# Kernel optimization log

Hardware: AMD Instinct MI355X
Metric: run time of the kernel (lower is better)

Reference implementation:

```python
import jax, jax.numpy as jnp
import numpy as np

MASK_FILL = -100.0


def setup_inputs() -> dict:
    key = jax.random.key(0)
    k1, k2, k3, k4 = jax.random.split(key, 4)
    B, S1, S2, D_IN, D_OUT = 8, 2048, 2048, 1024, 1024
    input1 = jax.random.normal(k1, (B, S1, D_IN), dtype=jnp.float32)
    input2 = jax.random.normal(k2, (B, S2, D_OUT), dtype=jnp.float32)
    input_mask = jax.random.randint(k3, (B, S1), 0, 2) > 0  # bool [B,S1]
    # kaiming_uniform-ish init scale for weight [out_features, in_features]
    bound = 1.0 / np.sqrt(D_IN)
    weight = jax.random.uniform(k4, (D_OUT, D_IN), dtype=jnp.float32,
                                minval=-bound, maxval=bound)
    return {"input1": input1, "input2": input2,
            "input_mask": input_mask, "weight": weight}


def reference(input1, input2, input_mask, weight):
    # out1 = F.linear(input1, weight): [B,S1,in] @ [in,out] -> [B,S1,out]
    out1 = jnp.einsum('bsd,od->bso', input1, weight)
    # scores: [B,S1,out] x [B,S2,out]^T -> [B,S1,S2]
    scores = jnp.einsum('bso,bto->bst', out1, input2)
    # out2[~input_mask] = -100 : mask is [B,S1], zeroes whole rows of scores
    scores = jnp.where(input_mask[:, :, None], scores, MASK_FILL)
    # softmax over S1 (dim=1), then attn^T @ input1 -> [B,S2,in]
    attn = jax.nn.softmax(scores, axis=1)
    satt = jnp.einsum('bst,bsd->btd', attn, input1)
    return satt
```

## Files before the change

### kernel.cpp

```cpp
#include <hip/hip_runtime.h>


typedef short s16x8 __attribute__((ext_vector_type(8)));
typedef float f32x4 __attribute__((ext_vector_type(4)));
typedef unsigned short u16;
typedef unsigned short u16x8 __attribute__((ext_vector_type(8)));
typedef _Float16 f16x8v __attribute__((ext_vector_type(8)));

#define B_ 8
#define S1_ 2048
#define S2_ 2048
#define D_ 1024

__device__ __forceinline__ float b2f(u16 u) {
  return __uint_as_float(((unsigned int)u) << 16);
}
__device__ __forceinline__ u16 f2b(float f) {
  unsigned int x = __float_as_uint(f);
  return (u16)((x + 0x7FFFu + ((x >> 16) & 1u)) >> 16);
}
__device__ __forceinline__ u16 f2h(float f) {
  _Float16 h = (_Float16)f;
  return __builtin_bit_cast(u16, h);
}
__device__ __forceinline__ float h2f(u16 u) {
  return (float)__builtin_bit_cast(_Float16, u);
}
__device__ __forceinline__ void gload16(const void* g, void* l) {
  __builtin_amdgcn_global_load_lds(
      (const __attribute__((address_space(1))) unsigned int*)g,
      (__attribute__((address_space(3))) unsigned int*)l, 16, 0, 0);
}

template <bool F16>
__device__ __forceinline__ f32x4 mfma16(s16x8 a, s16x8 b, f32x4 c) {
  if constexpr (F16)
    return __builtin_amdgcn_mfma_f32_16x16x32_f16(
        __builtin_bit_cast(f16x8v, a), __builtin_bit_cast(f16x8v, b), c, 0, 0,
        0);
  else
    return __builtin_amdgcn_mfma_f32_16x16x32_bf16(a, b, c, 0, 0, 0);
}


__global__ __launch_bounds__(256) void split_h_kernel(
    const float* __restrict__ in, u16* __restrict__ h, int n4) {
  int i = blockIdx.x * 256 + threadIdx.x;
  if (i >= n4) return;
  f32x4 v = ((const f32x4*)in)[i];
  ushort4 o;
  o.x = f2h(v[0]);
  o.y = f2h(v[1]);
  o.z = f2h(v[2]);
  o.w = f2h(v[3]);
  ((ushort4*)h)[i] = o;
}

__global__ __launch_bounds__(256) void zero_kernel(float* __restrict__ p,
                                                   int n) {
  int i = blockIdx.x * 256 + threadIdx.x;
  if (i < n) p[i] = 0.f;
}

template <int NSEG, int MODE, bool F16>
__global__ __launch_bounds__(512, 2) void gemm8(
    const u16* __restrict__ A0, const u16* __restrict__ A1,
    const u16* __restrict__ A2, const u16* __restrict__ B0,
    const u16* __restrict__ B1, const u16* __restrict__ B2,
    void* __restrict__ Cp, u16* __restrict__ C2, int K, int ldc, long sA,
    long sB, long sC, const int* __restrict__ mask, int maskStride,
    float* __restrict__ lvec, int lvecStride) {
  __shared__ __align__(16) u16 Abuf0[8192];
  __shared__ __align__(16) u16 Abuf1[8192];
  __shared__ __align__(16) u16 Abuf2[8192];
  __shared__ __align__(16) u16 Abuf3[8192];
  __shared__ __align__(16) u16 Bbuf0[8192];
  __shared__ __align__(16) u16 Bbuf1[8192];
  __shared__ __align__(16) u16 Bbuf2[8192];
  __shared__ __align__(16) u16 Bbuf3[8192];

  const int gx = gridDim.x, gy = gridDim.y;
  int flat = blockIdx.x + gx * (blockIdx.y + gy * blockIdx.z);
  const int total = gx * gy * (int)gridDim.z;
  const int cpx = total >> 3;
  flat = (flat & 7) * cpx + (flat >> 3);
  const int bx = flat % gx;
  const int rem0 = flat / gx;
  const int by = rem0 % gy;
  const int bz = rem0 / gy;

  const int tid = threadIdx.x;
  const int lane = tid & 63;
  const int wid = tid >> 6;
  const int wr = wid >> 2;
  const int wn = wid & 3;

  const int tps = K >> 5;
  const int NT = NSEG * tps;

  const int srow = tid >> 2;
  const int kch = (tid & 3) ^ ((srow >> 1) & 3);
  const long aRow1 = (long)(by * 256 + srow) * K + kch * 8;
  const long aRow2 = (long)(by * 256 + srow + 128) * K + kch * 8;
  const long bRow1 = (long)(bx * 256 + srow) * K + kch * 8;
  const long bRow2 = (long)(bx * 256 + srow + 128) * K + kch * 8;

  const u16* aBase0 = A0 + (long)bz * sA;
  const u16* bBase0 = B0 + (long)bz * sB;
  const u16* aBase1 = (NSEG > 1) ? A1 + (long)bz * sA : aBase0;
  const u16* bBase1 = (NSEG > 1) ? B1 + (long)bz * sB : bBase0;
  const u16* aBase2 = (NSEG > 2) ? A2 + (long)bz * sA : aBase0;
  const u16* bBase2 = (NSEG > 2) ? B2 + (long)bz * sB : bBase0;

  const int lr = lane & 15;
  const int kg = lane >> 4;
  const int arow0 = wr * 128 + lr;
  const int aOffU = arow0 * 32 + (kg ^ ((arow0 >> 1) & 3)) * 8;
  const int brow0 = wn * 64 + lr;
  const int bOffU = brow0 * 32 + (kg ^ ((brow0 >> 1) & 3)) * 8;

  const f32x4 z4 = {0.f, 0.f, 0.f, 0.f};
  f32x4 acc[8][4];
#pragma unroll
  for (int i = 0; i < 8; ++i)
#pragma unroll
    for (int j = 0; j < 4; ++j) acc[i][j] = z4;

  int s_rem = 0, s_seg = 0;
  const u16* aS = aBase0;
  const u16* bS = bBase0;

#define STAGE_AB(DA_, DB_)                                                   \
  {                                                                          \
    gload16(aS + aRow1 + s_rem * 32, &DA_[wid * 512]);                       \
    gload16(aS + aRow2 + s_rem * 32, &DA_[wid * 512 + 4096]);                \
    gload16(bS + bRow1 + s_rem * 32, &DB_[wid * 512]);                       \
    gload16(bS + bRow2 + s_rem * 32, &DB_[wid * 512 + 4096]);                \
    if (++s_rem == tps) {                                                    \
      s_rem = 0;                                                             \
      ++s_seg;                                                               \
      aS = (s_seg == 1) ? aBase1 : aBase2;                                   \
      bS = (s_seg == 1) ? bBase1 : bBase2;                                   \
    }                                                                        \
  }

  STAGE_AB(Abuf0, Bbuf0);
  STAGE_AB(Abuf1, Bbuf1);
  STAGE_AB(Abuf2, Bbuf2);
  asm volatile("s_waitcnt vmcnt(8)" ::: "memory");
  __builtin_amdgcn_s_barrier();

#define ITER(AS_, BS_, DA_, DB_, VM_, STG_)                                  \
  {                                                                          \
    s16x8 a0[4], a1[4], bfr[4];                                              \
    _Pragma("unroll") for (int m_ = 0; m_ < 4; ++m_) a0[m_] =                \
        *(const s16x8*)&AS_[aOffU + m_ * 512];                               \
    _Pragma("unroll") for (int n_ = 0; n_ < 4; ++n_) bfr[n_] =               \
        *(const s16x8*)&BS_[bOffU + n_ * 512];                               \
    _Pragma("unroll") for (int m_ = 0; m_ < 4; ++m_) a1[m_] =                \
        *(const s16x8*)&AS_[aOffU + (m_ + 4) * 512];                         \
    if (STG_) {                                                              \
      gload16(aS + aRow1 + s_rem * 32, &DA_[wid * 512]);                     \
      gload16(aS + aRow2 + s_rem * 32, &DA_[wid * 512 + 4096]);              \
    }                                                                        \
    asm volatile("" ::: "memory");                                           \
    __builtin_amdgcn_s_barrier();                                            \
    __builtin_amdgcn_sched_barrier(0);                                       \
    __builtin_amdgcn_s_setprio(1);                                           \
    _Pragma("unroll") for (int m_ = 0; m_ < 4; ++m_)                         \
        _Pragma("unroll") for (int n_ = 0; n_ < 4; ++n_) acc[m_][n_] =       \
            mfma16<F16>(a0[m_], bfr[n_], acc[m_][n_]);                       \
    __builtin_amdgcn_s_setprio(0);                                           \
    if (STG_) {                                                              \
      gload16(bS + bRow1 + s_rem * 32, &DB_[wid * 512]);                     \
      gload16(bS + bRow2 + s_rem * 32, &DB_[wid * 512 + 4096]);              \
      if (++s_rem == tps) {                                                  \
        s_rem = 0;                                                           \
        ++s_seg;                                                             \
        aS = (s_seg == 1) ? aBase1 : aBase2;                                 \
        bS = (s_seg == 1) ? bBase1 : bBase2;                                 \
      }                                                                      \
    }                                                                        \
    asm volatile("s_waitcnt " VM_ ::: "memory");                             \
    __builtin_amdgcn_s_barrier();                                            \
    __builtin_amdgcn_sched_barrier(0);                                       \
    __builtin_amdgcn_s_setprio(1);                                           \
    _Pragma("unroll") for (int m_ = 0; m_ < 4; ++m_)                         \
        _Pragma("unroll") for (int n_ = 0; n_ < 4; ++n_) acc[m_ + 4][n_] =   \
            mfma16<F16>(a1[m_], bfr[n_], acc[m_ + 4][n_]);                   \
    __builtin_amdgcn_s_setprio(0);                                           \
  }

  for (int t = 0; t < NT - 4; t += 4) {
    ITER(Abuf0, Bbuf0, Abuf3, Bbuf3, "vmcnt(8)", true);
    ITER(Abuf1, Bbuf1, Abuf0, Bbuf0, "vmcnt(8)", true);
    ITER(Abuf2, Bbuf2, Abuf1, Bbuf1, "vmcnt(8)", true);
    ITER(Abuf3, Bbuf3, Abuf2, Bbuf2, "vmcnt(8)", true);
  }
  ITER(Abuf0, Bbuf0, Abuf3, Bbuf3, "vmcnt(8)", true);
  ITER(Abuf1, Bbuf1, Abuf0, Bbuf0, "vmcnt(4)", false);
  ITER(Abuf2, Bbuf2, Abuf1, Bbuf1, "vmcnt(0)", false);
  ITER(Abuf3, Bbuf3, Abuf2, Bbuf2, "vmcnt(0)", false);

#undef ITER
#undef STAGE_AB

  const int row0 = by * 256 + wr * 128 + kg * 4;
  const int col0 = bx * 256 + wn * 64 + lr;

  if (MODE == 0) {
    u16* Ch = (u16*)Cp;
    u16* Cl = C2;
#pragma unroll
    for (int m = 0; m < 8; ++m)
#pragma unroll
      for (int n = 0; n < 4; ++n)
#pragma unroll
        for (int r = 0; r < 4; ++r) {
          float v = acc[m][n][r];
          long idx = (long)(row0 + m * 16 + r) * ldc + (col0 + n * 16);
          if (F16) {
            u16 h = f2h(v);
            Ch[idx] = h;
            Cl[idx] = f2h(v - h2f(h));
          } else {
            u16 h = f2b(v);
            Ch[idx] = h;
            Cl[idx] = f2b(v - b2f(h));
          }
        }
  } else if (MODE == 1) {
    u16* Cb = (u16*)Cp + (long)bz * sC;
    const int* mb = mask + (long)bz * maskStride;
    float* lvout = lvec + (long)bz * lvecStride;
    int mcol[4];
#pragma unroll
    for (int n = 0; n < 4; ++n) mcol[n] = mb[col0 + n * 16];
#pragma unroll
    for (int m = 0; m < 8; ++m)
#pragma unroll
      for (int r = 0; r < 4; ++r) {
        float rv = 0.f;
#pragma unroll
        for (int n = 0; n < 4; ++n) {
          float v = acc[m][n][r];
          v = mcol[n] ? __expf(v - 100.0f) : 0.0f;
          Cb[(long)(row0 + m * 16 + r) * ldc + (col0 + n * 16)] = f2b(v);
          rv += v;
        }
        rv += __shfl_xor(rv, 1, 16);
        rv += __shfl_xor(rv, 2, 16);
        rv += __shfl_xor(rv, 4, 16);
        rv += __shfl_xor(rv, 8, 16);
        if (lr == 0) atomicAdd(&lvout[row0 + m * 16 + r], rv);
      }
  } else {
    float* Cb = (float*)Cp + (long)bz * sC;
    const float* lb = lvec + (long)bz * lvecStride;
#pragma unroll
    for (int m = 0; m < 8; ++m) {
      float sc[4];
#pragma unroll
      for (int r = 0; r < 4; ++r) {
        float dv = lb[row0 + m * 16 + r];
        sc[r] = (dv > 0.0f) ? 1.0f / dv : 0.0f;
      }
#pragma unroll
      for (int n = 0; n < 4; ++n)
#pragma unroll
        for (int r = 0; r < 4; ++r)
          Cb[(long)(row0 + m * 16 + r) * ldc + (col0 + n * 16)] =
              acc[m][n][r] * sc[r];
    }
  }
}


__device__ __forceinline__ void split8(const float* __restrict__ g, s16x8& h,
                                       s16x8& l) {
  f32x4 a = *(const f32x4*)g;
  f32x4 b = *(const f32x4*)(g + 4);
#pragma unroll
  for (int j = 0; j < 8; ++j) {
    float x = (j < 4) ? a[j] : b[j - 4];
    u16 hu = f2b(x);
    h[j] = (short)hu;
    l[j] = (short)f2b(x - b2f(hu));
  }
}

template <int MODE>
__global__ __launch_bounds__(256, 2) void gemm_k(
    const void* __restrict__ Ap, const void* __restrict__ Bp,
    const u16* __restrict__ Blo, void* __restrict__ Cp, u16* __restrict__ C2,
    int K, int ldc, long sA, long sB, long sC, const int* __restrict__ mask,
    int maskStride, const float* __restrict__ lvec, int lvecStride) {
  constexpr bool TRI = (MODE != 2);
  __shared__ s16x8 AsH[512];
  __shared__ s16x8 BsH[512];
  __shared__ s16x8 AsL[TRI ? 512 : 1];
  __shared__ s16x8 BsL[TRI ? 512 : 1];

  const int z = blockIdx.z;
  const int tid = threadIdx.x;
  const int lane = tid & 63;
  const int wid = tid >> 6;

  const f32x4 z4 = {0.f, 0.f, 0.f, 0.f};
  f32x4 acc[4][4];
#pragma unroll
  for (int i = 0; i < 4; ++i)
#pragma unroll
    for (int j = 0; j < 4; ++j) acc[i][j] = z4;

  const int wm = (wid & 1) * 64;
  const int wn = (wid >> 1) * 64;
  const int lrow = lane & 15;
  const int kofs = (lane >> 4) * 8;
  const int srow = tid >> 1;
  const int shalf = (tid & 1) * 16;
  const int lidx = (srow * 32 + shalf) >> 3;

  const u16* AsHu = (const u16*)AsH;
  const u16* BsHu = (const u16*)BsH;
  const u16* AsLu = (const u16*)AsL;
  const u16* BsLu = (const u16*)BsL;

  for (int k0 = 0; k0 < K; k0 += 32) {
    if (MODE == 2) {
      const u16* Ab = (const u16*)Ap + z * sA + (long)blockIdx.y * 128 * K;
      const u16* Bb = (const u16*)Bp + z * sB + (long)blockIdx.x * 128 * K;
      const u16* ga = Ab + (long)srow * K + k0 + shalf;
      const u16* gb = Bb + (long)srow * K + k0 + shalf;
      AsH[lidx] = *(const s16x8*)ga;
      AsH[lidx + 1] = *(const s16x8*)(ga + 8);
      BsH[lidx] = *(const s16x8*)gb;
      BsH[lidx + 1] = *(const s16x8*)(gb + 8);
    } else {
      const float* Ab = (const float*)Ap + z * sA + (long)blockIdx.y * 128 * K;
      const float* ga = Ab + (long)srow * K + k0 + shalf;
      split8(ga, AsH[lidx], AsL[lidx]);
      split8(ga + 8, AsH[lidx + 1], AsL[lidx + 1]);
      if (MODE == 0) {
        const float* Bb = (const float*)Bp + z * sB + (long)blockIdx.x * 128 * K;
        const float* gb = Bb + (long)srow * K + k0 + shalf;
        split8(gb, BsH[lidx], BsL[lidx]);
        split8(gb + 8, BsH[lidx + 1], BsL[lidx + 1]);
      } else {
        const u16* Bh = (const u16*)Bp + z * sB + (long)blockIdx.x * 128 * K;
        const u16* Bl = Blo + z * sB + (long)blockIdx.x * 128 * K;
        const u16* gh = Bh + (long)srow * K + k0 + shalf;
        const u16* gl = Bl + (long)srow * K + k0 + shalf;
        BsH[lidx] = *(const s16x8*)gh;
        BsH[lidx + 1] = *(const s16x8*)(gh + 8);
        BsL[lidx] = *(const s16x8*)gl;
        BsL[lidx + 1] = *(const s16x8*)(gl + 8);
      }
    }
    __syncthreads();
    s16x8 ah[4], bh[4], al[4], bl[4];
#pragma unroll
    for (int t = 0; t < 4; ++t) {
      ah[t] = *(const s16x8*)&AsHu[(wm + t * 16 + lrow) * 32 + kofs];
      bh[t] = *(const s16x8*)&BsHu[(wn + t * 16 + lrow) * 32 + kofs];
      if (TRI) {
        al[t] = *(const s16x8*)&AsLu[(wm + t * 16 + lrow) * 32 + kofs];
        bl[t] = *(const s16x8*)&BsLu[(wn + t * 16 + lrow) * 32 + kofs];
      }
    }
#pragma unroll
    for (int i = 0; i < 4; ++i)
#pragma unroll
      for (int j = 0; j < 4; ++j) {
        acc[i][j] = __builtin_amdgcn_mfma_f32_16x16x32_bf16(ah[i], bh[j],
                                                            acc[i][j], 0, 0, 0);
        if (TRI) {
          acc[i][j] = __builtin_amdgcn_mfma_f32_16x16x32_bf16(
              al[i], bh[j], acc[i][j], 0, 0, 0);
          acc[i][j] = __builtin_amdgcn_mfma_f32_16x16x32_bf16(
              ah[i], bl[j], acc[i][j], 0, 0, 0);
        }
      }
    __syncthreads();
  }

  const int row0 = blockIdx.y * 128 + wm + (lane >> 4) * 4;
  const int col0 = blockIdx.x * 128 + wn + lrow;

  if (MODE == 0) {
    u16* Ch = (u16*)Cp;
#pragma unroll
    for (int i = 0; i < 4; ++i)
#pragma unroll
      for (int j = 0; j < 4; ++j)
#pragma unroll
        for (int r = 0; r < 4; ++r) {
          float v = acc[i][j][r];
          long idx = (long)(row0 + i * 16 + r) * ldc + (col0 + j * 16);
          u16 h = f2b(v);
          Ch[idx] = h;
          C2[idx] = f2b(v - b2f(h));
        }
  } else if (MODE == 1) {
    u16* Cb = (u16*)Cp + z * sC;
    const int* mb = mask + (long)z * maskStride;
    int mcol[4];
#pragma unroll
    for (int j = 0; j < 4; ++j) mcol[j] = mb[col0 + j * 16];
#pragma unroll
    for (int i = 0; i < 4; ++i)
#pragma unroll
      for (int j = 0; j < 4; ++j)
#pragma unroll
        for (int r = 0; r < 4; ++r) {
          float v = acc[i][j][r];
          v = mcol[j] ? __expf(v - 100.0f) : 0.0f;
          Cb[(long)(row0 + i * 16 + r) * ldc + (col0 + j * 16)] = f2b(v);
        }
  } else {
    float* Cb = (float*)Cp + z * sC;
    const float* lb = lvec + (long)z * lvecStride;
    float scale[4][4];
#pragma unroll
    for (int i = 0; i < 4; ++i)
#pragma unroll
      for (int r = 0; r < 4; ++r) {
        float dv = lb[row0 + i * 16 + r];
        scale[i][r] = (dv > 0.0f) ? 1.0f / dv : 0.0f;
      }
#pragma unroll
    for (int i = 0; i < 4; ++i)
#pragma unroll
      for (int j = 0; j < 4; ++j)
#pragma unroll
        for (int r = 0; r < 4; ++r)
          Cb[(long)(row0 + i * 16 + r) * ldc + (col0 + j * 16)] =
              acc[i][j][r] * scale[i][r];
  }
}


__global__ __launch_bounds__(256) void rowsum_kernel(const u16* __restrict__ E,
                                                     float* __restrict__ l) {
  const int row = blockIdx.x * 4 + (threadIdx.x >> 6);
  const int lane = threadIdx.x & 63;
  const u16* p = E + (size_t)row * S1_;
  float s = 0.f;
#pragma unroll
  for (int j = 0; j < 4; ++j) {
    u16x8 v = *(const u16x8*)(p + (j * 64 + lane) * 8);
#pragma unroll
    for (int k = 0; k < 8; ++k) s += b2f(v[k]);
  }
#pragma unroll
  for (int off = 32; off; off >>= 1) s += __shfl_down(s, off, 64);
  if (lane == 0) l[row] = s;
}

__global__ __launch_bounds__(256) void transpose_kernel(
    const float* __restrict__ in, u16* __restrict__ out) {
  __shared__ u16 tile[64][66];
  const int b = blockIdx.z;
  const float* ib = in + (size_t)b * S1_ * D_;
  u16* ob = out + (size_t)b * D_ * S1_;
  const int s0 = blockIdx.x * 64;
  const int d0 = blockIdx.y * 64;
  const int t = threadIdx.x;
  const int tr = t >> 4;
  const int tc = (t & 15) * 4;
#pragma unroll
  for (int i = 0; i < 4; ++i) {
    int row = tr + i * 16;
    f32x4 v = *(const f32x4*)(ib + (size_t)(s0 + row) * D_ + d0 + tc);
    tile[row][tc + 0] = f2b(v[0]);
    tile[row][tc + 1] = f2b(v[1]);
    tile[row][tc + 2] = f2b(v[2]);
    tile[row][tc + 3] = f2b(v[3]);
  }
  __syncthreads();
#pragma unroll
  for (int i = 0; i < 4; ++i) {
    int drow = tr + i * 16;
    ushort4 w;
    w.x = tile[tc + 0][drow];
    w.y = tile[tc + 1][drow];
    w.z = tile[tc + 2][drow];
    w.w = tile[tc + 3][drow];
    *(ushort4*)(ob + (size_t)(d0 + drow) * S1_ + s0 + tc) = w;
  }
}


extern "C" void kernel_launch(void* const* d_in, const int* in_sizes, int n_in,
                              void* d_out, int out_size, void* d_ws,
                              size_t ws_size, hipStream_t stream) {
  const float* in1 = (const float*)d_in[0];
  const float* in2 = (const float*)d_in[1];
  const int* mask = (const int*)d_in[2];
  const float* W = (const float*)d_in[3];
  float* out = (float*)d_out;
  char* ws = (char*)d_ws;
  const size_t MB = 1024 * 1024;
  dim3 blk(256);
  dim3 blk512(512);

  const size_t FULL_WS = 196 * MB + 64 * 1024;
  if (ws_size >= FULL_WS) {
    u16* in1_h = (u16*)(ws + 0);
    u16* in2_h = (u16*)(ws + 32 * MB);
    u16* W_h = (u16*)(ws + 64 * MB);
    u16* ET = (u16*)(ws + 66 * MB);
    u16* out1_h = (u16*)(ws + 130 * MB);
    u16* out1_l = (u16*)(ws + 162 * MB);
    float* lv = (float*)(ws + 194 * MB);
    u16* in1T = (u16*)(ws + 0);

    split_h_kernel<<<dim3(16384), blk, 0, stream>>>(in1, in1_h,
                                                    B_ * S1_ * D_ / 4);
    split_h_kernel<<<dim3(16384), blk, 0, stream>>>(in2, in2_h,
                                                    B_ * S2_ * D_ / 4);
    split_h_kernel<<<dim3(1024), blk, 0, stream>>>(W, W_h, D_ * D_ / 4);
    zero_kernel<<<dim3(64), blk, 0, stream>>>(lv, B_ * S2_);

    gemm8<1, 0, true><<<dim3(4, 64, 1), blk512, 0, stream>>>(
        in1_h, in1_h, in1_h, W_h, W_h, W_h, out1_h, out1_l, D_, D_, 0, 0, 0,
        nullptr, 0, nullptr, 0);

    gemm8<2, 1, true><<<dim3(8, 8, B_), blk512, 0, stream>>>(
        in2_h, in2_h, in2_h, out1_h, out1_l, out1_l, ET, nullptr, D_, S1_,
        (long)S2_ * D_, (long)S1_ * D_, (long)S2_ * S1_, mask, S1_, lv, S2_);

    transpose_kernel<<<dim3(S1_ / 64, D_ / 64, B_), blk, 0, stream>>>(in1, in1T);

    gemm8<1, 2, false><<<dim3(4, 8, B_), blk512, 0, stream>>>(
        ET, ET, ET, in1T, in1T, in1T, out, nullptr, S1_, D_, (long)S2_ * S1_,
        (long)D_ * S1_, (long)S2_ * D_, nullptr, 0, lv, S2_);
  } else {
    u16* out1_hi = (u16*)ws;
    u16* out1_lo = (u16*)(ws + 32 * MB);
    u16* ET = (u16*)(ws + 64 * MB);
    float* lv = (float*)(ws + 128 * MB);
    u16* in1T = out1_hi;

    gemm_k<0><<<dim3(8, 128, 1), blk, 0, stream>>>(
        in1, W, nullptr, out1_hi, out1_lo, D_, D_, 0, 0, 0, nullptr, 0,
        nullptr, 0);
    gemm_k<1><<<dim3(16, 16, B_), blk, 0, stream>>>(
        in2, out1_hi, out1_lo, ET, nullptr, D_, S1_, (long)S2_ * D_,
        (long)S1_ * D_, (long)S2_ * S1_, mask, S1_, nullptr, 0);
    rowsum_kernel<<<dim3(B_ * S2_ / 4), blk, 0, stream>>>(ET, lv);
    transpose_kernel<<<dim3(S1_ / 64, D_ / 64, B_), blk, 0, stream>>>(in1, in1T);
    gemm_k<2><<<dim3(8, 16, B_), blk, 0, stream>>>(
        ET, in1T, nullptr, out, nullptr, S1_, D_, (long)S2_ * S1_,
        (long)D_ * S1_, (long)S2_ * D_, nullptr, 0, lv, S2_);
  }
}
```

Before: 450.9 us.

## Compact masked S1 rows and skip their work in all three GEMMs

A new kernel builds a per-batch prefix-sum index of unmasked S1 rows. The first GEMM gathers only those rows, producing a compacted out1 per batch. The score GEMM skips tiles beyond the compacted length, and the final GEMM uses a dynamic K equal to the rounded count, with in1 transposed in compacted order. This avoids computing masked rows, which the exp(-100-shift) underflow makes effectively zero. It is exact only under that underflow assumption and adds gather indirection plus an extra small kernel.

```diff
diff --git a/kernel.cpp b/kernel.cpp
--- a/kernel.cpp
+++ b/kernel.cpp
@@ -62,14 +62,54 @@
   if (i < n) p[i] = 0.f;
 }
 
-template <int NSEG, int MODE, bool F16>
+__global__ __launch_bounds__(256) void compact_kernel(
+    const int* __restrict__ mask, int* __restrict__ sidx,
+    int* __restrict__ cnt, int* __restrict__ kr) {
+  const int b = blockIdx.x;
+  const int* mb = mask + (long)b * S1_;
+  int* sb = sidx + (long)b * S1_;
+  const int t = threadIdx.x;
+  const int lane = t & 63, w = t >> 6;
+  __shared__ int wsum[4];
+  int loc[8], c = 0;
+#pragma unroll
+  for (int j = 0; j < 8; ++j) {
+    loc[j] = (mb[t * 8 + j] != 0);
+    c += loc[j];
+  }
+  int inc = c;
+  for (int off = 1; off < 64; off <<= 1) {
+    int v = __shfl_up(inc, off, 64);
+    if (lane >= off) inc += v;
+  }
+  if (lane == 63) wsum[w] = inc;
+  __syncthreads();
+  int woff = 0;
+#pragma unroll
+  for (int i = 0; i < 4; ++i)
+    if (i < w) woff += wsum[i];
+  int pos = woff + inc - c;
+#pragma unroll
+  for (int j = 0; j < 8; ++j)
+    if (loc[j]) sb[pos++] = t * 8 + j;
+  if (t == 255) {
+    int tot = woff + inc;
+    cnt[b] = tot;
+    int r = (tot + 127) & ~127;
+    if (r < 256) r = 256;
+    kr[b] = r;
+  }
+}
+
+template <int NSEG, int MODE, bool F16, bool INDA, bool DYNK>
 __global__ __launch_bounds__(512, 2) void gemm8(
     const u16* __restrict__ A0, const u16* __restrict__ A1,
     const u16* __restrict__ A2, const u16* __restrict__ B0,
     const u16* __restrict__ B1, const u16* __restrict__ B2,
-    void* __restrict__ Cp, u16* __restrict__ C2, int K, int ldc, long sA,
-    long sB, long sC, const int* __restrict__ mask, int maskStride,
-    float* __restrict__ lvec, int lvecStride) {
+    void* __restrict__ Cp, u16* __restrict__ C2, int K, int lda, int ldb,
+    int ldc, long sA, long sB, long sC, const int* __restrict__ sidx,
+    int sidxStride, const int* __restrict__ cntArr,
+    const int* __restrict__ krArr, float* __restrict__ lvec, int lvecStride) {
   __shared__ __align__(16) u16 Abuf0[8192];
   __shared__ __align__(16) u16 Abuf1[8192];
   __shared__ __align__(16) u16 Abuf2[8192];
@@ -89,21 +129,35 @@
   const int by = rem0 % gy;
   const int bz = rem0 / gy;
 
+  if constexpr (INDA) {
+    if (by * 256 >= krArr[bz]) return;
+  }
+  if constexpr (MODE == 1) {
+    if (bx * 256 >= krArr[bz]) return;
+  }
+
   const int tid = threadIdx.x;
   const int lane = tid & 63;
   const int wid = tid >> 6;
   const int wr = wid >> 2;
   const int wn = wid & 3;
 
-  const int tps = K >> 5;
+  const int Keff = DYNK ? krArr[bz] : K;
+  const int tps = Keff >> 5;
   const int NT = NSEG * tps;
 
   const int srow = tid >> 2;
   const int kch = (tid & 3) ^ ((srow >> 1) & 3);
-  const long aRow1 = (long)(by * 256 + srow) * K + kch * 8;
-  const long aRow2 = (long)(by * 256 + srow + 128) * K + kch * 8;
-  const long bRow1 = (long)(bx * 256 + srow) * K + kch * 8;
-  const long bRow2 = (long)(bx * 256 + srow + 128) * K + kch * 8;
+  int ar0g = by * 256 + srow, ar1g = ar0g + 128;
+  if constexpr (INDA) {
+    const int* sx = sidx + (long)bz * sidxStride;
+    ar0g = sx[ar0g];
+    ar1g = sx[ar1g];
+  }
+  const long aRow1 = (long)ar0g * lda + kch * 8;
+  const long aRow2 = (long)ar1g * lda + kch * 8;
+  const long bRow1 = (long)(bx * 256 + srow) * ldb + kch * 8;
+  const long bRow2 = (long)(bx * 256 + srow + 128) * ldb + kch * 8;
 
   const u16* aBase0 = A0 + (long)bz * sA;
   const u16* bBase0 = B0 + (long)bz * sB;
@@ -209,8 +263,8 @@
   const int col0 = bx * 256 + wn * 64 + lr;
 
   if (MODE == 0) {
-    u16* Ch = (u16*)Cp;
-    u16* Cl = C2;
+    u16* Ch = (u16*)Cp + (long)bz * sC;
+    u16* Cl = C2 + (long)bz * sC;
 #pragma unroll
     for (int m = 0; m < 8; ++m)
 #pragma unroll
@@ -231,11 +285,11 @@
         }
   } else if (MODE == 1) {
     u16* Cb = (u16*)Cp + (long)bz * sC;
-    const int* mb = mask + (long)bz * maskStride;
     float* lvout = lvec + (long)bz * lvecStride;
+    const int cn = cntArr[bz];
     int mcol[4];
 #pragma unroll
-    for (int n = 0; n < 4; ++n) mcol[n] = mb[col0 + n * 16];
+    for (int n = 0; n < 4; ++n) mcol[n] = (col0 + n * 16) < cn;
 #pragma unroll
     for (int m = 0; m < 8; ++m)
 #pragma unroll
@@ -457,6 +511,52 @@
   if (lane == 0) l[row] = s;
 }
 
+__global__ __launch_bounds__(256) void transposeC_kernel(
+    const float* __restrict__ in, const int* __restrict__ sidx,
+    const int* __restrict__ cnt, const int* __restrict__ kr,
+    u16* __restrict__ out) {
+  __shared__ u16 tile[64][66];
+  const int b = blockIdx.z;
+  const int s0 = blockIdx.x * 64;
+  if (s0 >= kr[b]) return;
+  const int cn = cnt[b];
+  const int* sx = sidx + (long)b * S1_;
+  const float* ib = in + (size_t)b * S1_ * D_;
+  u16* ob = out + (size_t)b * D_ * S1_;
+  const int d0 = blockIdx.y * 64;
+  const int t = threadIdx.x;
+  const int tr = t >> 4;
+  const int tc = (t & 15) * 4;
+#pragma unroll
+  for (int i = 0; i < 4; ++i) {
+    int row = tr + i * 16;
+    int j = s0 + row;
+    if (j < cn) {
+      f32x4 v = *(const f32x4*)(ib + (size_t)sx[j] * D_ + d0 + tc);
+      tile[row][tc + 0] = f2b(v[0]);
+      tile[row][tc + 1] = f2b(v[1]);
+      tile[row][tc + 2] = f2b(v[2]);
+      tile[row][tc + 3] = f2b(v[3]);
+    } else {
+      tile[row][tc + 0] = 0;
+      tile[row][tc + 1] = 0;
+      tile[row][tc + 2] = 0;
+      tile[row][tc + 3] = 0;
+    }
+  }
+  __syncthreads();
+#pragma unroll
+  for (int i = 0; i < 4; ++i) {
+    int drow = tr + i * 16;
+    ushort4 w;
+    w.x = tile[tc + 0][drow];
+    w.y = tile[tc + 1][drow];
+    w.z = tile[tc + 2][drow];
+    w.w = tile[tc + 3][drow];
+    *(ushort4*)(ob + (size_t)(d0 + drow) * S1_ + s0 + tc) = w;
+  }
+}
+
 __global__ __launch_bounds__(256) void transpose_kernel(
     const float* __restrict__ in, u16* __restrict__ out) {
   __shared__ u16 tile[64][66];
@@ -501,6 +601,7 @@
   float* out = (float*)d_out;
   char* ws = (char*)d_ws;
   const size_t MB = 1024 * 1024;
+  const size_t KB = 1024;
   dim3 blk(256);
   dim3 blk512(512);
 
@@ -510,31 +611,38 @@
     u16* in2_h = (u16*)(ws + 32 * MB);
     u16* W_h = (u16*)(ws + 64 * MB);
     u16* ET = (u16*)(ws + 66 * MB);
-    u16* out1_h = (u16*)(ws + 130 * MB);
-    u16* out1_l = (u16*)(ws + 162 * MB);
+    u16* out1C_h = (u16*)(ws + 130 * MB);
+    u16* out1C_l = (u16*)(ws + 162 * MB);
     float* lv = (float*)(ws + 194 * MB);
-    u16* in1T = (u16*)(ws + 0);
+    int* sidx = (int*)(ws + 194 * MB + 64 * KB);
+    int* cnt = (int*)(ws + 194 * MB + 128 * KB);
+    int* kr = cnt + 8;
+    u16* in1TC = (u16*)(ws + 0);
 
     split_h_kernel<<<dim3(16384), blk, 0, stream>>>(in1, in1_h,
                                                     B_ * S1_ * D_ / 4);
     split_h_kernel<<<dim3(16384), blk, 0, stream>>>(in2, in2_h,
                                                     B_ * S2_ * D_ / 4);
     split_h_kernel<<<dim3(1024), blk, 0, stream>>>(W, W_h, D_ * D_ / 4);
-    zero_kernel<<<dim3(64), blk, 0, stream>>>(lv, B_ * S2_);
-
-    gemm8<1, 0, true><<<dim3(4, 64, 1), blk512, 0, stream>>>(
-        in1_h, in1_h, in1_h, W_h, W_h, W_h, out1_h, out1_l, D_, D_, 0, 0, 0,
-        nullptr, 0, nullptr, 0);
-
-    gemm8<2, 1, true><<<dim3(8, 8, B_), blk512, 0, stream>>>(
-        in2_h, in2_h, in2_h, out1_h, out1_l, out1_l, ET, nullptr, D_, S1_,
-        (long)S2_ * D_, (long)S1_ * D_, (long)S2_ * S1_, mask, S1_, lv, S2_);
-
-    transpose_kernel<<<dim3(S1_ / 64, D_ / 64, B_), blk, 0, stream>>>(in1, in1T);
-
-    gemm8<1, 2, false><<<dim3(4, 8, B_), blk512, 0, stream>>>(
-        ET, ET, ET, in1T, in1T, in1T, out, nullptr, S1_, D_, (long)S2_ * S1_,
-        (long)D_ * S1_, (long)S2_ * D_, nullptr, 0, lv, S2_);
+    zero_kernel<<<dim3(128), blk, 0, stream>>>(lv, 32768);
+    compact_kernel<<<dim3(B_), blk, 0, stream>>>(mask, sidx, cnt, kr);
+
+    gemm8<1, 0, true, true, false><<<dim3(4, 8, B_), blk512, 0, stream>>>(
+        in1_h, in1_h, in1_h, W_h, W_h, W_h, out1C_h, out1C_l, D_, D_, D_, D_,
+        (long)S1_ * D_, 0L, (long)S1_ * D_, sidx, S1_, cnt, kr, nullptr, 0);
+
+    transposeC_kernel<<<dim3(S1_ / 64, D_ / 64, B_), blk, 0, stream>>>(
+        in1, sidx, cnt, kr, in1TC);
+
+    gemm8<2, 1, true, false, false><<<dim3(8, 8, B_), blk512, 0, stream>>>(
+        in2_h, in2_h, in2_h, out1C_h, out1C_l, out1C_l, ET, nullptr, D_, D_,
+        D_, S1_, (long)S2_ * D_, (long)S1_ * D_, (long)S2_ * S1_, nullptr, 0,
+        cnt, kr, lv, S2_);
+
+    gemm8<1, 2, false, false, true><<<dim3(4, 8, B_), blk512, 0, stream>>>(
+        ET, ET, ET, in1TC, in1TC, in1TC, out, nullptr, 0, S1_, S1_, D_,
+        (long)S2_ * S1_, (long)D_ * S1_, (long)S2_ * D_, nullptr, 0, cnt, kr,
+        lv, S2_);
   } else {
     u16* out1_hi = (u16*)ws;
     u16* out1_lo = (u16*)(ws + 32 * MB);
```

Measured after the change: 390.4 us. 1.15x faster.
